# Kernel tuning notes

Measured on AMD Instinct MI355X. Metric: run time of the kernel, lower is better.

The kernel has to match this reference:

```python
import jax, jax.numpy as jnp
import numpy as np

DIM = 256
NH = 4
HD = DIM // NH
RR = 8
EPS_BN = 1e-5


def dwconv(x, w, b):
    # depthwise conv, stride 1, SAME padding (odd kernel, pad=k//2)
    out = jax.lax.conv_general_dilated(
        x, w, window_strides=(1, 1), padding='SAME',
        feature_group_count=x.shape[1],
        dimension_numbers=('NCHW', 'OIHW', 'NCHW'))
    return out + b[None, :, None, None]


def conv1x1(x, w, b):
    # w: [out_c, in_c]
    return jnp.einsum('bchw,oc->bohw', x, w) + b[None, :, None, None]


def bn_eval(x, g, be, m, v):
    inv = g / jnp.sqrt(v + EPS_BN)
    return x * inv[None, :, None, None] + (be - m * inv)[None, :, None, None]


def l2norm(x):
    n = jnp.sqrt(jnp.sum(x * x, axis=-1, keepdims=True))
    return x / jnp.maximum(n, 1e-12)


def setup_inputs() -> dict:
    key = jax.random.key(0)
    ks = jax.random.split(key, 32)
    d = {}
    d['x1'] = jax.random.normal(ks[0], (8, DIM, 64, 64), jnp.float32)
    d['x2'] = jax.random.normal(ks[1], (8, DIM, 64, 64), jnp.float32)
    # multi-scale depthwise convs k=3,5,7
    for i, k in enumerate([3, 5, 7]):
        d[f'ms_w{k}'] = jax.random.normal(ks[2 + i], (DIM, 1, k, k), jnp.float32) * (1.0 / k)
        d[f'ms_b{k}'] = jax.random.normal(ks[5 + i], (DIM,), jnp.float32) * 0.02
    # qkv 1x1 conv + BN params for each stream
    for s, off in [(1, 8), (2, 16)]:
        d[f'qkv{s}_w'] = jax.random.normal(ks[off], (3 * DIM, DIM), jnp.float32) * (DIM ** -0.5)
        d[f'qkv{s}_b'] = jnp.zeros((3 * DIM,), jnp.float32)
        d[f'bn{s}_g'] = 1.0 + 0.1 * jax.random.normal(ks[off + 1], (3 * DIM,), jnp.float32)
        d[f'bn{s}_b'] = 0.1 * jax.random.normal(ks[off + 2], (3 * DIM,), jnp.float32)
        d[f'bn{s}_m'] = 0.1 * jax.random.normal(ks[off + 3], (3 * DIM,), jnp.float32)
        d[f'bn{s}_v'] = jax.random.uniform(ks[off + 4], (3 * DIM,), jnp.float32, 0.5, 1.5)
    # SE channel attention (shared module)
    d['ca_w1'] = jax.random.normal(ks[24], (DIM // RR, DIM), jnp.float32) * (DIM ** -0.5)
    d['ca_b1'] = jnp.zeros((DIM // RR,), jnp.float32)
    d['ca_w2'] = jax.random.normal(ks[25], (DIM, DIM // RR), jnp.float32) * ((DIM // RR) ** -0.5)
    d['ca_b2'] = jnp.zeros((DIM,), jnp.float32)
    # output projections
    d['po1_w'] = jax.random.normal(ks[26], (DIM, DIM), jnp.float32) * (DIM ** -0.5)
    d['po1_b'] = jnp.zeros((DIM,), jnp.float32)
    d['po2_w'] = jax.random.normal(ks[27], (DIM, DIM), jnp.float32) * (DIM ** -0.5)
    d['po2_b'] = jnp.zeros((DIM,), jnp.float32)
    return d


def _scfa(x1, x2, ms_w3, ms_b3, ms_w5, ms_b5, ms_w7, ms_b7,
          qkv1_w, qkv1_b, bn1_g, bn1_b, bn1_m, bn1_v,
          qkv2_w, qkv2_b, bn2_g, bn2_b, bn2_m, bn2_v,
          ca_w1, ca_b1, ca_w2, ca_b2, po1_w, po1_b, po2_w, po2_b):
    b, c, h, w = x1.shape
    temp = HD ** -0.5

    def multi_scale(x):
        return (dwconv(x, ms_w3, ms_b3) + dwconv(x, ms_w5, ms_b5) + dwconv(x, ms_w7, ms_b7)) / 3.0

    x1f = multi_scale(x1)
    x2f = multi_scale(x2)

    qkv1 = jax.nn.gelu(bn_eval(conv1x1(x1f, qkv1_w, qkv1_b), bn1_g, bn1_b, bn1_m, bn1_v), approximate=False)
    qkv2 = jax.nn.gelu(bn_eval(conv1x1(x2f, qkv2_w, qkv2_b), bn2_g, bn2_b, bn2_m, bn2_v), approximate=False)

    def split_heads(t):
        q, k, v = jnp.split(t, 3, axis=1)
        f = lambda z: z.reshape(b, NH, HD, h * w)
        return f(q), f(k), f(v)

    x1_q, x1_k, x1_v = split_heads(qkv1)
    x2_q, x2_k, x2_v = split_heads(qkv2)

    q1, k2 = l2norm(x1_q), l2norm(x2_k)
    q2, k1 = l2norm(x2_q), l2norm(x1_k)

    attn1 = jax.nn.softmax(jnp.einsum('bhcn,bhdn->bhcd', q1, k2) * temp, axis=-1)
    attn2 = jax.nn.softmax(jnp.einsum('bhcn,bhdn->bhcd', q2, k1) * temp, axis=-1)

    x1_out = jnp.einsum('bhcd,bhdn->bhcn', attn1, x1_v).reshape(b, c, h, w)
    x2_out = jnp.einsum('bhcd,bhdn->bhcn', attn2, x2_v).reshape(b, c, h, w)

    def se_gate(x):
        p = x.mean(axis=(2, 3))  # [b, c]
        y = jax.nn.relu(jnp.einsum('bc,rc->br', p, ca_w1) + ca_b1)
        y = jax.nn.sigmoid(jnp.einsum('br,cr->bc', y, ca_w2) + ca_b2)
        return y[:, :, None, None]

    x1_out = x1_out * se_gate(x1_out)
    x2_out = x2_out * se_gate(x2_out)

    x1_out = conv1x1(x1_out, po1_w, po1_b) + x1
    x2_out = conv1x1(x2_out, po2_w, po2_b) + x2
    return x1_out, x2_out


def reference(x1, x2, ms_w3, ms_b3, ms_w5, ms_b5, ms_w7, ms_b7,
              qkv1_w, qkv1_b, bn1_g, bn1_b, bn1_m, bn1_v,
              qkv2_w, qkv2_b, bn2_g, bn2_b, bn2_m, bn2_v,
              ca_w1, ca_b1, ca_w2, ca_b2, po1_w, po1_b, po2_w, po2_b):
    return _scfa(x1, x2, ms_w3, ms_b3, ms_w5, ms_b5, ms_w7, ms_b7,
                 qkv1_w, qkv1_b, bn1_g, bn1_b, bn1_m, bn1_v,
                 qkv2_w, qkv2_b, bn2_g, bn2_b, bn2_m, bn2_v,
                 ca_w1, ca_b1, ca_w2, ca_b2, po1_w, po1_b, po2_w, po2_b)
```

## Files before the change

kernel.cpp:

```cpp
#include <hip/hip_runtime.h>
#include <hip/hip_bf16.h>


#define NPIX 4096

typedef __attribute__((ext_vector_type(8))) short bfrag;
typedef __attribute__((ext_vector_type(4))) float f4acc;

#define GLDS16(g, l) __builtin_amdgcn_global_load_lds( \
    (const __attribute__((address_space(1))) unsigned int*)(g), \
    (__attribute__((address_space(3))) unsigned int*)(l), 16, 0, 0)

__device__ __forceinline__ float bf2f(unsigned short h) {
  return __uint_as_float(((unsigned)h) << 16);
}
__device__ __forceinline__ unsigned short f2bf(float f) {
  unsigned u = __float_as_uint(f);
  unsigned r = (u + 0x7FFFu + ((u >> 16) & 1u)) >> 16;
  return (unsigned short)r;
}
__device__ __forceinline__ float gelu_f(float x) {
  float z = x * (1.5957691216f + 0.0713548163f * x * x);
  return x / (1.0f + __expf(-z));
}

__global__ __launch_bounds__(256) void prep_kernel(
    const float* __restrict__ w3, const float* __restrict__ b3,
    const float* __restrict__ w5, const float* __restrict__ b5,
    const float* __restrict__ w7, const float* __restrict__ b7,
    const float* __restrict__ qb1, const float* __restrict__ g1,
    const float* __restrict__ be1, const float* __restrict__ m1,
    const float* __restrict__ v1,
    const float* __restrict__ qb2, const float* __restrict__ g2,
    const float* __restrict__ be2, const float* __restrict__ m2,
    const float* __restrict__ v2,
    float* __restrict__ weff, float* __restrict__ beff,
    float* __restrict__ alpha, float* __restrict__ beta)
{
  const int c = threadIdx.x;
  for (int ky = 0; ky < 7; ++ky)
    for (int kx = 0; kx < 7; ++kx) {
      float w = w7[c * 49 + ky * 7 + kx];
      if (ky >= 1 && ky <= 5 && kx >= 1 && kx <= 5)
        w += w5[c * 25 + (ky - 1) * 5 + (kx - 1)];
      if (ky >= 2 && ky <= 4 && kx >= 2 && kx <= 4)
        w += w3[c * 9 + (ky - 2) * 3 + (kx - 2)];
      weff[c * 49 + ky * 7 + kx] = w * (1.0f / 3.0f);
    }
  beff[c] = (b3[c] + b5[c] + b7[c]) * (1.0f / 3.0f);
  for (int o = c; o < 768; o += 256) {
    float inv1 = g1[o] / sqrtf(v1[o] + 1e-5f);
    alpha[o] = inv1;
    beta[o]  = qb1[o] * inv1 + be1[o] - m1[o] * inv1;
    float inv2 = g2[o] / sqrtf(v2[o] + 1e-5f);
    alpha[768 + o] = inv2;
    beta[768 + o]  = qb2[o] * inv2 + be2[o] - m2[o] * inv2;
  }
}

__global__ __launch_bounds__(256) void convert_w(
    const float* __restrict__ s1, const float* __restrict__ s2,
    unsigned short* __restrict__ d1, unsigned short* __restrict__ d2)
{
  int idx = blockIdx.x * 256 + threadIdx.x;
  d1[idx] = f2bf(s1[idx]);
  d2[idx] = f2bf(s2[idx]);
}

__global__ __launch_bounds__(256) void ms_conv(
    const float* __restrict__ x1, const float* __restrict__ x2,
    const float* __restrict__ weff, const float* __restrict__ beff,
    unsigned short* __restrict__ xf0, unsigned short* __restrict__ xf1)
{
  __shared__ float tile[70][76];
  const int bc2 = blockIdx.x;
  const int s = bc2 >> 11, bc = bc2 & 2047;
  const int c = bc & 255;
  const int tid = threadIdx.x;
  const float* src = (s ? x2 : x1) + (size_t)bc * NPIX;
  float wreg[49];
#pragma unroll
  for (int i = 0; i < 49; ++i) wreg[i] = weff[c * 49 + i];
  const float bias = beff[c];
  for (int idx = tid; idx < 70 * 76; idx += 256) {
    int ry = idx / 76, cx = idx - ry * 76;
    int gy = ry - 3, gx = cx - 4;
    float v = 0.0f;
    if ((unsigned)gy < 64u && (unsigned)gx < 64u) v = src[gy * 64 + gx];
    tile[ry][cx] = v;
  }
  __syncthreads();
  const int x0 = (tid & 15) * 4;
  const int y0 = (tid >> 4) * 4;
  float acc[4][4];
#pragma unroll
  for (int yo = 0; yo < 4; ++yo)
#pragma unroll
    for (int xo = 0; xo < 4; ++xo) acc[yo][xo] = bias;
#pragma unroll
  for (int r = 0; r < 10; ++r) {
    float seg[12];
    *(float4*)&seg[0] = *(const float4*)&tile[y0 + r][x0];
    *(float4*)&seg[4] = *(const float4*)&tile[y0 + r][x0 + 4];
    *(float4*)&seg[8] = *(const float4*)&tile[y0 + r][x0 + 8];
    const int yolo = (r >= 6) ? (r - 6) : 0;
    const int yohi = (r < 3) ? r : 3;
#pragma unroll
    for (int yo = 0; yo < 4; ++yo) {
      if (yo < yolo || yo > yohi) continue;
      const int ky = r - yo;
#pragma unroll
      for (int kx = 0; kx < 7; ++kx) {
        const float w = wreg[ky * 7 + kx];
#pragma unroll
        for (int xo = 0; xo < 4; ++xo)
          acc[yo][xo] = fmaf(w, seg[1 + xo + kx], acc[yo][xo]);
      }
    }
  }
  unsigned short* dst = (s ? xf1 : xf0) + (size_t)bc * NPIX;
#pragma unroll
  for (int yo = 0; yo < 4; ++yo) {
    ushort4 u;
    u.x = f2bf(acc[yo][0]); u.y = f2bf(acc[yo][1]);
    u.z = f2bf(acc[yo][2]); u.w = f2bf(acc[yo][3]);
    *(ushort4*)&dst[(y0 + yo) * 64 + x0] = u;
  }
}

__global__ __launch_bounds__(256) void transpose_bf16(
    const unsigned short* __restrict__ s0, unsigned short* __restrict__ d0,
    const unsigned short* __restrict__ s1, unsigned short* __restrict__ d1,
    long sb, long db)
{
  __shared__ unsigned short T[64][72];
  const int n0 = blockIdx.x * 64, c0 = blockIdx.y * 64;
  const int z = blockIdx.z, st = z >> 3, b = z & 7;
  const unsigned short* src = st ? s1 : s0;
  unsigned short* dst = st ? d1 : d0;
  const int t = threadIdx.x;
  const int rhi = t >> 4, c4 = (t & 15) * 4;
#pragma unroll
  for (int rr = 0; rr < 4; ++rr) {
    int row = rr * 16 + rhi;
    ushort4 u = *(const ushort4*)&src[(size_t)b * sb + (size_t)(c0 + row) * NPIX + n0 + c4];
    T[row][c4 + 0] = u.x; T[row][c4 + 1] = u.y;
    T[row][c4 + 2] = u.z; T[row][c4 + 3] = u.w;
  }
  __syncthreads();
#pragma unroll
  for (int rr = 0; rr < 4; ++rr) {
    int nrow = rr * 16 + rhi;
    ushort4 u;
    u.x = T[c4 + 0][nrow]; u.y = T[c4 + 1][nrow];
    u.z = T[c4 + 2][nrow]; u.w = T[c4 + 3][nrow];
    *(ushort4*)&dst[(size_t)b * db + (size_t)(n0 + nrow) * 256 + c0 + c4] = u;
  }
}

__global__ __launch_bounds__(256) void qkv_gemm(
    const unsigned short* __restrict__ W1, const unsigned short* __restrict__ W2,
    const unsigned short* __restrict__ X0, const unsigned short* __restrict__ X1,
    const float* __restrict__ alpha, const float* __restrict__ beta,
    unsigned short* __restrict__ q1, unsigned short* __restrict__ q2,
    float* __restrict__ ns)
{
  __shared__ unsigned short As[2][128 * 64];
  __shared__ unsigned short Bs[2][128 * 64];
  const int n0 = blockIdx.x * 128, o0 = blockIdx.y * 128;
  const int z = blockIdx.z, s = z >> 3, b = z & 7;
  const unsigned short* Wb = s ? W2 : W1;
  const unsigned short* Xt = s ? X1 : X0;
  unsigned short* qkv = s ? q2 : q1;
  const float* al = alpha + s * 768;
  const float* be = beta + s * 768;
  float* normsq = ns + s * 4096;
  const int tid = threadIdx.x, w = tid >> 6, lane = tid & 63;
  const int wm = (w & 1) * 64;
  const int wn = (w >> 1) * 64;
  const int lrow8 = lane >> 3;
  const int lcolsw = ((lane & 7) ^ lrow8) * 8;
  const int fslot = lane & 7;
  f4acc acc[4][4] = {};
  auto stage = [&](int buf, int kc) {
#pragma unroll
    for (int j = 0; j < 4; ++j) {
      int i = w * 4 + j;
      GLDS16(Wb + (size_t)(o0 + i * 8 + lrow8) * 256 + kc + lcolsw, &As[buf][i * 512]);
      GLDS16(Xt + (size_t)b * 1048576 + (size_t)(n0 + i * 8 + lrow8) * 256 + kc + lcolsw,
             &Bs[buf][i * 512]);
    }
  };
  stage(0, 0);
#pragma unroll
  for (int t = 0; t < 4; ++t) {
    const int cur = t & 1;
    if (t < 3) stage(cur ^ 1, (t + 1) * 64);
    if (t < 3) asm volatile("s_waitcnt vmcnt(8)" ::: "memory");
    else       asm volatile("s_waitcnt vmcnt(0)" ::: "memory");
    __builtin_amdgcn_s_barrier();
#pragma unroll
    for (int ks = 0; ks < 2; ++ks) {
      const int slot = ((ks * 4 + (lane >> 4)) ^ fslot) * 8;
      bfrag a[4], bb[4];
#pragma unroll
      for (int mt = 0; mt < 4; ++mt)
        a[mt] = *(const bfrag*)&Bs[cur][(wm + mt * 16 + (lane & 15)) * 64 + slot];
#pragma unroll
      for (int nt = 0; nt < 4; ++nt)
        bb[nt] = *(const bfrag*)&As[cur][(wn + nt * 16 + (lane & 15)) * 64 + slot];
#pragma unroll
      for (int mt = 0; mt < 4; ++mt)
#pragma unroll
        for (int nt = 0; nt < 4; ++nt)
          acc[mt][nt] = __builtin_amdgcn_mfma_f32_16x16x32_bf16(a[mt], bb[nt], acc[mt][nt], 0, 0, 0);
    }
    __builtin_amdgcn_s_barrier();
  }
#pragma unroll
  for (int nt = 0; nt < 4; ++nt) {
    const int o = o0 + wn + nt * 16 + (lane & 15);
    const float alv = al[o], bev = be[o];
    unsigned short* orow = qkv + ((size_t)b * 768 + o) * NPIX;
    float sq = 0.0f;
#pragma unroll
    for (int mt = 0; mt < 4; ++mt) {
      const int n = n0 + wm + mt * 16 + (lane >> 4) * 4;
      float v0 = gelu_f(acc[mt][nt][0] * alv + bev);
      float v1 = gelu_f(acc[mt][nt][1] * alv + bev);
      float v2 = gelu_f(acc[mt][nt][2] * alv + bev);
      float v3 = gelu_f(acc[mt][nt][3] * alv + bev);
      ushort4 u;
      u.x = f2bf(v0); u.y = f2bf(v1); u.z = f2bf(v2); u.w = f2bf(v3);
      *(ushort4*)&orow[n] = u;
      sq += v0 * v0 + v1 * v1 + v2 * v2 + v3 * v3;
    }
    if (o0 + wn + nt * 16 < 512) {
      sq += __shfl_xor(sq, 16);
      sq += __shfl_xor(sq, 32);
      if (lane < 16) atomicAdd(&normsq[b * 512 + o], sq);
    }
  }
}

__global__ __launch_bounds__(256) void spart_kernel(
    const unsigned short* __restrict__ qkv1, const unsigned short* __restrict__ qkv2,
    float* __restrict__ Sp0, float* __restrict__ Sp1)
{
  __shared__ unsigned short Qs[2][64 * 128];
  __shared__ unsigned short Ks[2][64 * 128];
  const int ck = blockIdx.x, h = blockIdx.y;
  const int z = blockIdx.z, s = z >> 3, b = z & 7;
  const unsigned short* qs = s ? qkv2 : qkv1;
  const unsigned short* kp = (s ? qkv1 : qkv2) + 256 * NPIX;
  float* Sp = s ? Sp1 : Sp0;
  const int tid = threadIdx.x, w = tid >> 6, lane = tid & 63;
  const int lrow16 = lane >> 4;
  const size_t qbase = ((size_t)b * 768 + h * 64) * NPIX;
  f4acc acc[4] = {};
  auto stage = [&](int buf, int it) {
    const int noff = ck * 512 + it * 128;
#pragma unroll
    for (int j = 0; j < 4; ++j) {
      int i = w * 4 + j;
      int row = i * 4 + lrow16;
      int colsw = ((lane & 15) ^ (row & 15)) * 8;
      GLDS16(qs + qbase + (size_t)row * NPIX + noff + colsw, &Qs[buf][i * 512]);
      GLDS16(kp + qbase + (size_t)row * NPIX + noff + colsw, &Ks[buf][i * 512]);
    }
  };
  stage(0, 0);
#pragma unroll
  for (int it = 0; it < 4; ++it) {
    const int cur = it & 1;
    if (it < 3) stage(cur ^ 1, it + 1);
    if (it < 3) asm volatile("s_waitcnt vmcnt(8)" ::: "memory");
    else        asm volatile("s_waitcnt vmcnt(0)" ::: "memory");
    __builtin_amdgcn_s_barrier();
#pragma unroll
    for (int kk = 0; kk < 4; ++kk) {
      const int slot = ((kk * 4 + (lane >> 4)) ^ (lane & 15)) * 8;
      bfrag bq = *(const bfrag*)&Qs[cur][(w * 16 + (lane & 15)) * 128 + slot];
#pragma unroll
      for (int mt = 0; mt < 4; ++mt) {
        bfrag ak = *(const bfrag*)&Ks[cur][(mt * 16 + (lane & 15)) * 128 + slot];
        acc[mt] = __builtin_amdgcn_mfma_f32_16x16x32_bf16(ak, bq, acc[mt], 0, 0, 0);
      }
    }
    __builtin_amdgcn_s_barrier();
  }
  float* dst = Sp + ((size_t)(ck * 32) + b * 4 + h) * 4096;
  const int c = w * 16 + (lane & 15);
#pragma unroll
  for (int mt = 0; mt < 4; ++mt)
    *(float4*)&dst[c * 64 + mt * 16 + (lane >> 4) * 4] = *(float4*)&acc[mt];
}

__global__ __launch_bounds__(256) void softattn(
    const float* __restrict__ Sp0, const float* __restrict__ Sp1,
    const float* __restrict__ ns,
    unsigned short* __restrict__ at0, unsigned short* __restrict__ at1)
{
  const int bh2 = blockIdx.x;
  const int s = bh2 >> 5, bh = bh2 & 31;
  const int b = bh >> 2, h = bh & 3;
  const float* Sp = s ? Sp1 : Sp0;
  const float* nsq = ns + s * 4096;
  const float* nsk = ns + (s ^ 1) * 4096;
  unsigned short* attn = s ? at1 : at0;
  const int wv = threadIdx.x >> 6, lane = threadIdx.x & 63;
  const float ikd = 1.0f / fmaxf(sqrtf(nsk[b * 512 + 256 + h * 64 + lane]), 1e-12f);
  for (int c = wv; c < 64; c += 4) {
    float sm = 0.0f;
#pragma unroll
    for (int ch = 0; ch < 8; ++ch)
      sm += Sp[((size_t)(ch * 32) + bh) * 4096 + c * 64 + lane];
    const float iq = 1.0f / fmaxf(sqrtf(nsq[b * 512 + h * 64 + c]), 1e-12f);
    float zv = sm * 0.125f * iq * ikd;
    float m = zv;
#pragma unroll
    for (int off = 32; off > 0; off >>= 1) m = fmaxf(m, __shfl_xor(m, off));
    float e = expf(zv - m);
    float sum = e;
#pragma unroll
    for (int off = 32; off > 0; off >>= 1) sum += __shfl_xor(sum, off);
    attn[(size_t)bh * 4096 + c * 64 + lane] = f2bf(e / sum);
  }
}

__global__ __launch_bounds__(256) void av_kernel(
    const unsigned short* __restrict__ vt0, const unsigned short* __restrict__ vt1,
    const unsigned short* __restrict__ at0, const unsigned short* __restrict__ at1,
    unsigned short* __restrict__ xo0, unsigned short* __restrict__ xo1,
    long db, float* __restrict__ pool)
{
  __shared__ unsigned short Vs[256 * 64];
  __shared__ unsigned short At[64 * 64];
  const int n0 = blockIdx.x * 256, h = blockIdx.y;
  const int z = blockIdx.z, s = z >> 3, b = z & 7;
  const unsigned short* vt = s ? vt1 : vt0;
  const unsigned short* attn = s ? at1 : at0;
  unsigned short* xout = s ? xo1 : xo0;
  float* pl = pool + s * 2048;
  const int tid = threadIdx.x, w = tid >> 6, lane = tid & 63;
  const int lrow8 = lane >> 3;
  const int lcolsw = ((lane & 7) ^ lrow8) * 8;
  const int bh = b * 4 + h;
#pragma unroll
  for (int j = 0; j < 8; ++j) {
    int i = w * 8 + j;
    GLDS16(vt + ((size_t)b * 1048576 + (size_t)(n0 + i * 8 + lrow8) * 256) + h * 64 + lcolsw,
           &Vs[i * 512]);
  }
#pragma unroll
  for (int j = 0; j < 2; ++j) {
    int i = w * 2 + j;
    GLDS16(attn + (size_t)bh * 4096 + (size_t)(i * 8 + lrow8) * 64 + lcolsw, &At[i * 512]);
  }
  __syncthreads();
  f4acc acc[4][4] = {};
#pragma unroll
  for (int ks = 0; ks < 2; ++ks) {
    const int slot = ((ks * 4 + (lane >> 4)) ^ (lane & 7)) * 8;
    bfrag a[4], bb[4];
#pragma unroll
    for (int mt = 0; mt < 4; ++mt)
      a[mt] = *(const bfrag*)&At[(mt * 16 + (lane & 15)) * 64 + slot];
#pragma unroll
    for (int nt = 0; nt < 4; ++nt)
      bb[nt] = *(const bfrag*)&Vs[(w * 64 + nt * 16 + (lane & 15)) * 64 + slot];
#pragma unroll
    for (int mt = 0; mt < 4; ++mt)
#pragma unroll
      for (int nt = 0; nt < 4; ++nt)
        acc[mt][nt] = __builtin_amdgcn_mfma_f32_16x16x32_bf16(a[mt], bb[nt], acc[mt][nt], 0, 0, 0);
  }
#pragma unroll
  for (int mt = 0; mt < 4; ++mt) {
    const int c = mt * 16 + (lane >> 4) * 4;
    float s0 = 0.0f, s1 = 0.0f, s2 = 0.0f, s3 = 0.0f;
#pragma unroll
    for (int nt = 0; nt < 4; ++nt) {
      const int np = n0 + w * 64 + nt * 16 + (lane & 15);
      ushort4 u;
      u.x = f2bf(acc[mt][nt][0]); u.y = f2bf(acc[mt][nt][1]);
      u.z = f2bf(acc[mt][nt][2]); u.w = f2bf(acc[mt][nt][3]);
      *(ushort4*)&xout[(size_t)b * db + (size_t)np * 256 + h * 64 + c] = u;
      s0 += acc[mt][nt][0]; s1 += acc[mt][nt][1];
      s2 += acc[mt][nt][2]; s3 += acc[mt][nt][3];
    }
    s0 += __shfl_xor(s0, 1); s0 += __shfl_xor(s0, 2); s0 += __shfl_xor(s0, 4); s0 += __shfl_xor(s0, 8);
    s1 += __shfl_xor(s1, 1); s1 += __shfl_xor(s1, 2); s1 += __shfl_xor(s1, 4); s1 += __shfl_xor(s1, 8);
    s2 += __shfl_xor(s2, 1); s2 += __shfl_xor(s2, 2); s2 += __shfl_xor(s2, 4); s2 += __shfl_xor(s2, 8);
    s3 += __shfl_xor(s3, 1); s3 += __shfl_xor(s3, 2); s3 += __shfl_xor(s3, 4); s3 += __shfl_xor(s3, 8);
    if ((lane & 15) == 0) {
      atomicAdd(&pl[b * 256 + h * 64 + c + 0], s0);
      atomicAdd(&pl[b * 256 + h * 64 + c + 1], s1);
      atomicAdd(&pl[b * 256 + h * 64 + c + 2], s2);
      atomicAdd(&pl[b * 256 + h * 64 + c + 3], s3);
    }
  }
}

__global__ __launch_bounds__(256) void segate_scale(
    const float* __restrict__ pool, const float* __restrict__ w1,
    const float* __restrict__ b1, const float* __restrict__ w2,
    const float* __restrict__ b2,
    const float* __restrict__ W1, const float* __restrict__ W2,
    unsigned short* __restrict__ Wg)
{
  const int b16 = blockIdx.x;
  const int tid = threadIdx.x;
  __shared__ float p[256];
  __shared__ float hh[32];
  p[tid] = pool[b16 * 256 + tid] * (1.0f / 4096.0f);
  __syncthreads();
  if (tid < 32) {
    float s = b1[tid];
    for (int c = 0; c < 256; ++c) s = fmaf(w1[tid * 256 + c], p[c], s);
    hh[tid] = fmaxf(s, 0.0f);
  }
  __syncthreads();
  float s = b2[tid];
#pragma unroll
  for (int r = 0; r < 32; ++r) s = fmaf(w2[tid * 32 + r], hh[r], s);
  const float g = 1.0f / (1.0f + expf(-s));
  const float* W = (b16 >> 3) ? W2 : W1;
  for (int o = 0; o < 256; ++o)
    Wg[(size_t)b16 * 65536 + o * 256 + tid] = f2bf(W[o * 256 + tid] * g);
}

__global__ __launch_bounds__(256) void pout_gemm(
    const unsigned short* __restrict__ Wgall,
    const unsigned short* __restrict__ X0, const unsigned short* __restrict__ X1,
    long db, const float* __restrict__ bias0, const float* __restrict__ bias1,
    const float* __restrict__ xr0, const float* __restrict__ xr1,
    float* __restrict__ out)
{
  __shared__ unsigned short As[2][128 * 64];
  __shared__ unsigned short Bs[2][128 * 64];
  const int n0 = blockIdx.x * 128, o0 = blockIdx.y * 128;
  const int z = blockIdx.z, s = z >> 3, b = z & 7;
  const unsigned short* Wg = Wgall + (size_t)z * 65536;
  const unsigned short* Xt = s ? X1 : X0;
  const float* bias = s ? bias1 : bias0;
  const float* xresb = s ? xr1 : xr0;
  float* outb = out + (size_t)s * 8388608;
  const int tid = threadIdx.x, w = tid >> 6, lane = tid & 63;
  const int wm = (w & 1) * 64;
  const int wn = (w >> 1) * 64;
  const int lrow8 = lane >> 3;
  const int lcolsw = ((lane & 7) ^ lrow8) * 8;
  const int fslot = lane & 7;
  f4acc acc[4][4] = {};
  auto stage = [&](int buf, int kc) {
#pragma unroll
    for (int j = 0; j < 4; ++j) {
      int i = w * 4 + j;
      GLDS16(Wg + (size_t)(o0 + i * 8 + lrow8) * 256 + kc + lcolsw, &As[buf][i * 512]);
      GLDS16(Xt + (size_t)b * db + (size_t)(n0 + i * 8 + lrow8) * 256 + kc + lcolsw,
             &Bs[buf][i * 512]);
    }
  };
  stage(0, 0);
#pragma unroll
  for (int t = 0; t < 4; ++t) {
    const int cur = t & 1;
    if (t < 3) stage(cur ^ 1, (t + 1) * 64);
    if (t < 3) asm volatile("s_waitcnt vmcnt(8)" ::: "memory");
    else       asm volatile("s_waitcnt vmcnt(0)" ::: "memory");
    __builtin_amdgcn_s_barrier();
#pragma unroll
    for (int ks = 0; ks < 2; ++ks) {
      const int slot = ((ks * 4 + (lane >> 4)) ^ fslot) * 8;
      bfrag a[4], bb[4];
#pragma unroll
      for (int mt = 0; mt < 4; ++mt)
        a[mt] = *(const bfrag*)&Bs[cur][(wm + mt * 16 + (lane & 15)) * 64 + slot];
#pragma unroll
      for (int nt = 0; nt < 4; ++nt)
        bb[nt] = *(const bfrag*)&As[cur][(wn + nt * 16 + (lane & 15)) * 64 + slot];
#pragma unroll
      for (int mt = 0; mt < 4; ++mt)
#pragma unroll
        for (int nt = 0; nt < 4; ++nt)
          acc[mt][nt] = __builtin_amdgcn_mfma_f32_16x16x32_bf16(a[mt], bb[nt], acc[mt][nt], 0, 0, 0);
    }
    __builtin_amdgcn_s_barrier();
  }
#pragma unroll
  for (int nt = 0; nt < 4; ++nt) {
    const int o = o0 + wn + nt * 16 + (lane & 15);
    const float bi = bias[o];
    const float* res = xresb + ((size_t)b * 256 + o) * NPIX;
    float* orow = outb + ((size_t)b * 256 + o) * NPIX;
#pragma unroll
    for (int mt = 0; mt < 4; ++mt) {
      const int n = n0 + wm + mt * 16 + (lane >> 4) * 4;
      float4 r4 = *(const float4*)&res[n];
      float4 ov;
      ov.x = acc[mt][nt][0] + bi + r4.x;
      ov.y = acc[mt][nt][1] + bi + r4.y;
      ov.z = acc[mt][nt][2] + bi + r4.z;
      ov.w = acc[mt][nt][3] + bi + r4.w;
      *(float4*)&orow[n] = ov;
    }
  }
}

extern "C" void kernel_launch(void* const* d_in, const int* in_sizes, int n_in,
                              void* d_out, int out_size, void* d_ws, size_t ws_size,
                              hipStream_t stream) {
  const float* x1    = (const float*)d_in[0];
  const float* x2    = (const float*)d_in[1];
  const float* ms_w3 = (const float*)d_in[2];
  const float* ms_b3 = (const float*)d_in[3];
  const float* ms_w5 = (const float*)d_in[4];
  const float* ms_b5 = (const float*)d_in[5];
  const float* ms_w7 = (const float*)d_in[6];
  const float* ms_b7 = (const float*)d_in[7];
  const float* qkv1_w = (const float*)d_in[8];
  const float* qkv1_b = (const float*)d_in[9];
  const float* bn1_g = (const float*)d_in[10];
  const float* bn1_b = (const float*)d_in[11];
  const float* bn1_m = (const float*)d_in[12];
  const float* bn1_v = (const float*)d_in[13];
  const float* qkv2_w = (const float*)d_in[14];
  const float* qkv2_b = (const float*)d_in[15];
  const float* bn2_g = (const float*)d_in[16];
  const float* bn2_b = (const float*)d_in[17];
  const float* bn2_m = (const float*)d_in[18];
  const float* bn2_v = (const float*)d_in[19];
  const float* ca_w1 = (const float*)d_in[20];
  const float* ca_b1 = (const float*)d_in[21];
  const float* ca_w2 = (const float*)d_in[22];
  const float* ca_b2 = (const float*)d_in[23];
  const float* po1_w = (const float*)d_in[24];
  const float* po1_b = (const float*)d_in[25];
  const float* po2_w = (const float*)d_in[26];
  const float* po2_b = (const float*)d_in[27];

  char* ws = (char*)d_ws;
  float* weff  = (float*)(ws + 0);
  float* beff  = (float*)(ws + 51200);
  float* alpha = (float*)(ws + 53248);
  float* beta  = (float*)(ws + 59392);
  float* normsq = (float*)(ws + 65536);
  float* pool  = (float*)(ws + 98304);
  unsigned short* W1b = (unsigned short*)(ws + 131072);
  unsigned short* W2b = (unsigned short*)(ws + 524288);
  unsigned short* Wg  = (unsigned short*)(ws + 917504);
  unsigned short* attn1 = (unsigned short*)(ws + 3014656);
  unsigned short* attn2 = (unsigned short*)(ws + 3276800);
  float* Sp    = (float*)(ws + 3538944);
  unsigned short* xf   = (unsigned short*)(ws + 7733248);
  unsigned short* xf_t = (unsigned short*)(ws + 24510464);
  unsigned short* qkv1 = (unsigned short*)(ws + 41287680);
  unsigned short* qkv2 = (unsigned short*)(ws + 91619328);
  unsigned short* xf2   = (unsigned short*)d_out;
  unsigned short* xf2_t = (unsigned short*)((char*)d_out + 16777216);
  float* Sp2 = (float*)(ws + 7733248);
  unsigned short* v1t   = xf;
  unsigned short* v2t   = xf_t;
  unsigned short* xout1 = qkv2;
  unsigned short* xout2 = qkv1;
  const long QKV_BSTR = 768L * 4096;

  float* outf = (float*)d_out;

  prep_kernel<<<1, 256, 0, stream>>>(ms_w3, ms_b3, ms_w5, ms_b5, ms_w7, ms_b7,
                                     qkv1_b, bn1_g, bn1_b, bn1_m, bn1_v,
                                     qkv2_b, bn2_g, bn2_b, bn2_m, bn2_v,
                                     weff, beff, alpha, beta);
  convert_w<<<768, 256, 0, stream>>>(qkv1_w, qkv2_w, W1b, W2b);
  hipMemsetAsync(ws + 65536, 0, 49152, stream);

  ms_conv<<<4096, 256, 0, stream>>>(x1, x2, weff, beff, xf, xf2);
  transpose_bf16<<<dim3(64, 4, 16), 256, 0, stream>>>(xf, xf_t, xf2, xf2_t,
                                                      1048576L, 1048576L);
  qkv_gemm<<<dim3(32, 6, 16), 256, 0, stream>>>(W1b, W2b, xf_t, xf2_t,
                                                alpha, beta, qkv1, qkv2, normsq);

  spart_kernel<<<dim3(8, 4, 16), 256, 0, stream>>>(qkv1, qkv2, Sp, Sp2);
  softattn<<<64, 256, 0, stream>>>(Sp, Sp2, normsq, attn1, attn2);

  transpose_bf16<<<dim3(64, 4, 16), 256, 0, stream>>>(qkv1 + 512 * NPIX, v1t,
                                                      qkv2 + 512 * NPIX, v2t,
                                                      3145728L, 1048576L);

  av_kernel<<<dim3(16, 4, 16), 256, 0, stream>>>(v1t, v2t, attn1, attn2,
                                                 xout1, xout2, QKV_BSTR, pool);

  segate_scale<<<16, 256, 0, stream>>>(pool, ca_w1, ca_b1, ca_w2, ca_b2,
                                       po1_w, po2_w, Wg);

  pout_gemm<<<dim3(32, 2, 16), 256, 0, stream>>>(Wg, xout1, xout2, QKV_BSTR,
                                                 po1_b, po2_b, x1, x2, outf);
}
```

Measured before the change: 422.4 us.

## Fuse transposes into ms_conv and qkv_gemm epilogues, removing transpose kernels

The multi-scale depthwise conv now processes 8 channels per block over a 16-row stripe and writes its bf16 output directly in pixel-major (transposed) layout, using lane shuffles to pack adjacent channels. The qkv GEMM swaps its MFMA operands for the V tiles so it can write V in transposed layout from the epilogue. Both standalone transpose_bf16 launches go away, saving their full read/write passes and two launches. The cost is 4-byte scattered stores with 512-byte stride in ms_conv, a branch in the GEMM inner loop, and workspace buffers remapped (Sp2 moved into the output buffer).

```diff
diff --git a/kernel.cpp b/kernel.cpp
--- a/kernel.cpp
+++ b/kernel.cpp
@@ -70,91 +70,96 @@
 __global__ __launch_bounds__(256) void ms_conv(
     const float* __restrict__ x1, const float* __restrict__ x2,
     const float* __restrict__ weff, const float* __restrict__ beff,
-    unsigned short* __restrict__ xf0, unsigned short* __restrict__ xf1)
-{
-  __shared__ float tile[70][76];
-  const int bc2 = blockIdx.x;
-  const int s = bc2 >> 11, bc = bc2 & 2047;
-  const int c = bc & 255;
+    unsigned short* __restrict__ xft0, unsigned short* __restrict__ xft1)
+{
+  __shared__ float tile[8 * 1584];
+  const int stripe = blockIdx.x;
+  const int oct = blockIdx.y;
+  const int z = blockIdx.z, s = z >> 3, b = z & 7;
+  const int c0 = oct * 8;
+  const float* xin = (s ? x2 : x1) + ((size_t)b * 256 + c0) * NPIX;
+  unsigned short* xft = (s ? xft1 : xft0) + (size_t)b * 1048576;
   const int tid = threadIdx.x;
-  const float* src = (s ? x2 : x1) + (size_t)bc * NPIX;
+  const int w = tid >> 6;
+  const int gy0 = stripe * 16 - 3;
+  for (int k = 0; k < 13; ++k) {
+    int idx = k * 256 + tid;
+    if (idx < 3168) {
+      int ch = idx / 396;
+      int rem = idx - ch * 396;
+      int ry = rem / 18;
+      int qx = rem - ry * 18;
+      int gy = gy0 + ry, gx = qx * 4 - 4;
+      if ((unsigned)gy < 64u && (unsigned)gx < 64u) {
+        GLDS16(xin + (size_t)ch * NPIX + gy * 64 + gx,
+               &tile[(k * 256 + w * 64) * 4]);
+      } else {
+        float4 zz = {0.0f, 0.0f, 0.0f, 0.0f};
+        *(float4*)&tile[idx * 4] = zz;
+      }
+    }
+  }
+  __syncthreads();
+  const int ch = tid & 7;
+  const int blk = tid >> 3;
+  const int x0 = (blk & 15) * 4;
+  const int ybase = (blk >> 4) * 4;
   float wreg[49];
 #pragma unroll
-  for (int i = 0; i < 49; ++i) wreg[i] = weff[c * 49 + i];
-  const float bias = beff[c];
-  for (int idx = tid; idx < 70 * 76; idx += 256) {
-    int ry = idx / 76, cx = idx - ry * 76;
-    int gy = ry - 3, gx = cx - 4;
-    float v = 0.0f;
-    if ((unsigned)gy < 64u && (unsigned)gx < 64u) v = src[gy * 64 + gx];
-    tile[ry][cx] = v;
-  }
-  __syncthreads();
-  const int x0 = (tid & 15) * 4;
-  const int y0 = (tid >> 4) * 4;
-  float acc[4][4];
-#pragma unroll
-  for (int yo = 0; yo < 4; ++yo)
-#pragma unroll
-    for (int xo = 0; xo < 4; ++xo) acc[yo][xo] = bias;
-#pragma unroll
-  for (int r = 0; r < 10; ++r) {
-    float seg[12];
-    *(float4*)&seg[0] = *(const float4*)&tile[y0 + r][x0];
-    *(float4*)&seg[4] = *(const float4*)&tile[y0 + r][x0 + 4];
-    *(float4*)&seg[8] = *(const float4*)&tile[y0 + r][x0 + 8];
-    const int yolo = (r >= 6) ? (r - 6) : 0;
-    const int yohi = (r < 3) ? r : 3;
+  for (int i = 0; i < 49; ++i) wreg[i] = weff[(c0 + ch) * 49 + i];
+  const float bias = beff[c0 + ch];
+  const float* trow = &tile[ch * 1584];
+#pragma unroll
+  for (int iter = 0; iter < 2; ++iter) {
+    const int Y0 = ybase + iter * 8;
+    float acc[4][4];
+#pragma unroll
+    for (int yo = 0; yo < 4; ++yo)
+#pragma unroll
+      for (int xo = 0; xo < 4; ++xo) acc[yo][xo] = bias;
+#pragma unroll
+    for (int r = 0; r < 10; ++r) {
+      float seg[12];
+      const int fidx = (Y0 + r) * 72 + x0;
+      *(float4*)&seg[0] = *(const float4*)&trow[fidx];
+      *(float4*)&seg[4] = *(const float4*)&trow[fidx + 4];
+      *(float4*)&seg[8] = *(const float4*)&trow[fidx + 8];
+      const int yolo = (r >= 6) ? (r - 6) : 0;
+      const int yohi = (r < 3) ? r : 3;
+#pragma unroll
+      for (int yo = 0; yo < 4; ++yo) {
+        if (yo < yolo || yo > yohi) continue;
+        const int ky = r - yo;
+#pragma unroll
+        for (int kx = 0; kx < 7; ++kx) {
+          const float wv = wreg[ky * 7 + kx];
+#pragma unroll
+          for (int xo = 0; xo < 4; ++xo)
+            acc[yo][xo] = fmaf(wv, seg[1 + xo + kx], acc[yo][xo]);
+        }
+      }
+    }
 #pragma unroll
     for (int yo = 0; yo < 4; ++yo) {
-      if (yo < yolo || yo > yohi) continue;
-      const int ky = r - yo;
-#pragma unroll
-      for (int kx = 0; kx < 7; ++kx) {
-        const float w = wreg[ky * 7 + kx];
-#pragma unroll
-        for (int xo = 0; xo < 4; ++xo)
-          acc[yo][xo] = fmaf(w, seg[1 + xo + kx], acc[yo][xo]);
+      const int n = (stripe * 16 + Y0 + yo) * 64 + x0;
+      unsigned p01 = (unsigned)f2bf(acc[yo][0]) | ((unsigned)f2bf(acc[yo][1]) << 16);
+      unsigned p23 = (unsigned)f2bf(acc[yo][2]) | ((unsigned)f2bf(acc[yo][3]) << 16);
+      unsigned o01 = (unsigned)__shfl_xor((int)p01, 1);
+      unsigned o23 = (unsigned)__shfl_xor((int)p23, 1);
+      unsigned w0, w1;
+      int off;
+      if (ch & 1) {
+        w0 = (o01 >> 16) | (p01 & 0xFFFF0000u);
+        w1 = (o23 >> 16) | (p23 & 0xFFFF0000u);
+        off = (n + 1) * 256 + c0 + ch - 1;
+      } else {
+        w0 = (p01 & 0xFFFFu) | (o01 << 16);
+        w1 = (p23 & 0xFFFFu) | (o23 << 16);
+        off = n * 256 + c0 + ch;
       }
-    }
-  }
-  unsigned short* dst = (s ? xf1 : xf0) + (size_t)bc * NPIX;
-#pragma unroll
-  for (int yo = 0; yo < 4; ++yo) {
-    ushort4 u;
-    u.x = f2bf(acc[yo][0]); u.y = f2bf(acc[yo][1]);
-    u.z = f2bf(acc[yo][2]); u.w = f2bf(acc[yo][3]);
-    *(ushort4*)&dst[(y0 + yo) * 64 + x0] = u;
-  }
-}
-
-__global__ __launch_bounds__(256) void transpose_bf16(
-    const unsigned short* __restrict__ s0, unsigned short* __restrict__ d0,
-    const unsigned short* __restrict__ s1, unsigned short* __restrict__ d1,
-    long sb, long db)
-{
-  __shared__ unsigned short T[64][72];
-  const int n0 = blockIdx.x * 64, c0 = blockIdx.y * 64;
-  const int z = blockIdx.z, st = z >> 3, b = z & 7;
-  const unsigned short* src = st ? s1 : s0;
-  unsigned short* dst = st ? d1 : d0;
-  const int t = threadIdx.x;
-  const int rhi = t >> 4, c4 = (t & 15) * 4;
-#pragma unroll
-  for (int rr = 0; rr < 4; ++rr) {
-    int row = rr * 16 + rhi;
-    ushort4 u = *(const ushort4*)&src[(size_t)b * sb + (size_t)(c0 + row) * NPIX + n0 + c4];
-    T[row][c4 + 0] = u.x; T[row][c4 + 1] = u.y;
-    T[row][c4 + 2] = u.z; T[row][c4 + 3] = u.w;
-  }
-  __syncthreads();
-#pragma unroll
-  for (int rr = 0; rr < 4; ++rr) {
-    int nrow = rr * 16 + rhi;
-    ushort4 u;
-    u.x = T[c4 + 0][nrow]; u.y = T[c4 + 1][nrow];
-    u.z = T[c4 + 2][nrow]; u.w = T[c4 + 3][nrow];
-    *(ushort4*)&dst[(size_t)b * db + (size_t)(n0 + nrow) * 256 + c0 + c4] = u;
+      *(unsigned*)&xft[off] = w0;
+      *(unsigned*)&xft[off + 512] = w1;
+    }
   }
 }
 
@@ -163,7 +168,8 @@
     const unsigned short* __restrict__ X0, const unsigned short* __restrict__ X1,
     const float* __restrict__ alpha, const float* __restrict__ beta,
     unsigned short* __restrict__ q1, unsigned short* __restrict__ q2,
-    float* __restrict__ ns)
+    float* __restrict__ ns,
+    unsigned short* __restrict__ v1t, unsigned short* __restrict__ v2t)
 {
   __shared__ unsigned short As[2][128 * 64];
   __shared__ unsigned short Bs[2][128 * 64];
@@ -175,6 +181,7 @@
   const float* al = alpha + s * 768;
   const float* be = beta + s * 768;
   float* normsq = ns + s * 4096;
+  const bool vsw = (o0 >= 512);
   const int tid = threadIdx.x, w = tid >> 6, lane = tid & 63;
   const int wm = (w & 1) * 64;
   const int wn = (w >> 1) * 64;
@@ -209,36 +216,66 @@
 #pragma unroll
       for (int nt = 0; nt < 4; ++nt)
         bb[nt] = *(const bfrag*)&As[cur][(wn + nt * 16 + (lane & 15)) * 64 + slot];
-#pragma unroll
-      for (int mt = 0; mt < 4; ++mt)
-#pragma unroll
-        for (int nt = 0; nt < 4; ++nt)
-          acc[mt][nt] = __builtin_amdgcn_mfma_f32_16x16x32_bf16(a[mt], bb[nt], acc[mt][nt], 0, 0, 0);
+      if (!vsw) {
+#pragma unroll
+        for (int mt = 0; mt < 4; ++mt)
+#pragma unroll
+          for (int nt = 0; nt < 4; ++nt)
+            acc[mt][nt] = __builtin_amdgcn_mfma_f32_16x16x32_bf16(a[mt], bb[nt], acc[mt][nt], 0, 0, 0);
+      } else {
+#pragma unroll
+        for (int mt = 0; mt < 4; ++mt)
+#pragma unroll
+          for (int nt = 0; nt < 4; ++nt)
+            acc[mt][nt] = __builtin_amdgcn_mfma_f32_16x16x32_bf16(bb[nt], a[mt], acc[mt][nt], 0, 0, 0);
+      }
     }
     __builtin_amdgcn_s_barrier();
   }
-#pragma unroll
-  for (int nt = 0; nt < 4; ++nt) {
-    const int o = o0 + wn + nt * 16 + (lane & 15);
-    const float alv = al[o], bev = be[o];
-    unsigned short* orow = qkv + ((size_t)b * 768 + o) * NPIX;
-    float sq = 0.0f;
-#pragma unroll
-    for (int mt = 0; mt < 4; ++mt) {
-      const int n = n0 + wm + mt * 16 + (lane >> 4) * 4;
-      float v0 = gelu_f(acc[mt][nt][0] * alv + bev);
-      float v1 = gelu_f(acc[mt][nt][1] * alv + bev);
-      float v2 = gelu_f(acc[mt][nt][2] * alv + bev);
-      float v3 = gelu_f(acc[mt][nt][3] * alv + bev);
-      ushort4 u;
-      u.x = f2bf(v0); u.y = f2bf(v1); u.z = f2bf(v2); u.w = f2bf(v3);
-      *(ushort4*)&orow[n] = u;
-      sq += v0 * v0 + v1 * v1 + v2 * v2 + v3 * v3;
-    }
-    if (o0 + wn + nt * 16 < 512) {
+  if (!vsw) {
+#pragma unroll
+    for (int nt = 0; nt < 4; ++nt) {
+      const int o = o0 + wn + nt * 16 + (lane & 15);
+      const float alv = al[o], bev = be[o];
+      unsigned short* orow = qkv + ((size_t)b * 768 + o) * NPIX;
+      float sq = 0.0f;
+#pragma unroll
+      for (int mt = 0; mt < 4; ++mt) {
+        const int n = n0 + wm + mt * 16 + (lane >> 4) * 4;
+        float v0 = gelu_f(acc[mt][nt][0] * alv + bev);
+        float v1 = gelu_f(acc[mt][nt][1] * alv + bev);
+        float v2 = gelu_f(acc[mt][nt][2] * alv + bev);
+        float v3 = gelu_f(acc[mt][nt][3] * alv + bev);
+        ushort4 u;
+        u.x = f2bf(v0); u.y = f2bf(v1); u.z = f2bf(v2); u.w = f2bf(v3);
+        *(ushort4*)&orow[n] = u;
+        sq += v0 * v0 + v1 * v1 + v2 * v2 + v3 * v3;
+      }
       sq += __shfl_xor(sq, 16);
       sq += __shfl_xor(sq, 32);
       if (lane < 16) atomicAdd(&normsq[b * 512 + o], sq);
+    }
+  } else {
+    unsigned short* vtb = (s ? v2t : v1t) + (size_t)b * 1048576;
+#pragma unroll
+    for (int nt = 0; nt < 4; ++nt) {
+      const int orr = wn + nt * 16 + (lane >> 4) * 4;
+      const int ob = o0 + orr;
+      const float a0 = al[ob + 0], b0 = be[ob + 0];
+      const float a1 = al[ob + 1], b1 = be[ob + 1];
+      const float a2 = al[ob + 2], b2 = be[ob + 2];
+      const float a3 = al[ob + 3], b3 = be[ob + 3];
+      const int c = (o0 - 512) + orr;
+#pragma unroll
+      for (int mt = 0; mt < 4; ++mt) {
+        const int n = n0 + wm + mt * 16 + (lane & 15);
+        ushort4 u;
+        u.x = f2bf(gelu_f(acc[mt][nt][0] * a0 + b0));
+        u.y = f2bf(gelu_f(acc[mt][nt][1] * a1 + b1));
+        u.z = f2bf(gelu_f(acc[mt][nt][2] * a2 + b2));
+        u.w = f2bf(gelu_f(acc[mt][nt][3] * a3 + b3));
+        *(ushort4*)&vtb[(size_t)n * 256 + c] = u;
+      }
     }
   }
 }
@@ -553,15 +590,13 @@
   unsigned short* attn1 = (unsigned short*)(ws + 3014656);
   unsigned short* attn2 = (unsigned short*)(ws + 3276800);
   float* Sp    = (float*)(ws + 3538944);
-  unsigned short* xf   = (unsigned short*)(ws + 7733248);
+  unsigned short* v1t  = (unsigned short*)(ws + 7733248);
   unsigned short* xf_t = (unsigned short*)(ws + 24510464);
   unsigned short* qkv1 = (unsigned short*)(ws + 41287680);
   unsigned short* qkv2 = (unsigned short*)(ws + 91619328);
-  unsigned short* xf2   = (unsigned short*)d_out;
+  unsigned short* v2t   = (unsigned short*)d_out;
   unsigned short* xf2_t = (unsigned short*)((char*)d_out + 16777216);
-  float* Sp2 = (float*)(ws + 7733248);
-  unsigned short* v1t   = xf;
-  unsigned short* v2t   = xf_t;
+  float* Sp2            = (float*)((char*)d_out + 33554432);
   unsigned short* xout1 = qkv2;
   unsigned short* xout2 = qkv1;
   const long QKV_BSTR = 768L * 4096;
@@ -575,19 +610,14 @@
   convert_w<<<768, 256, 0, stream>>>(qkv1_w, qkv2_w, W1b, W2b);
   hipMemsetAsync(ws + 65536, 0, 49152, stream);
 
-  ms_conv<<<4096, 256, 0, stream>>>(x1, x2, weff, beff, xf, xf2);
-  transpose_bf16<<<dim3(64, 4, 16), 256, 0, stream>>>(xf, xf_t, xf2, xf2_t,
-                                                      1048576L, 1048576L);
+  ms_conv<<<dim3(4, 32, 16), 256, 0, stream>>>(x1, x2, weff, beff, xf_t, xf2_t);
   qkv_gemm<<<dim3(32, 6, 16), 256, 0, stream>>>(W1b, W2b, xf_t, xf2_t,
-                                                alpha, beta, qkv1, qkv2, normsq);
+                                                alpha, beta, qkv1, qkv2, normsq,
+                                                v1t, v2t);
 
   spart_kernel<<<dim3(8, 4, 16), 256, 0, stream>>>(qkv1, qkv2, Sp, Sp2);
   softattn<<<64, 256, 0, stream>>>(Sp, Sp2, normsq, attn1, attn2);
 
-  transpose_bf16<<<dim3(64, 4, 16), 256, 0, stream>>>(qkv1 + 512 * NPIX, v1t,
-                                                      qkv2 + 512 * NPIX, v2t,
-                                                      3145728L, 1048576L);
-
   av_kernel<<<dim3(16, 4, 16), 256, 0, stream>>>(v1t, v2t, attn1, attn2,
                                                  xout1, xout2, QKV_BSTR, pool);
 
```

After: 467.4 us. 10.7% more time.
